# Kernel tuning notes

Measured on AMD Instinct MI355X. Metric: run time of the kernel, lower is better.

Reference implementation:

```python
import jax, jax.numpy as jnp
import numpy as np

N = 10000
E = 160000
SDIM = 256
VDIM = 128
EDIM = 32
GDIM = 32
NRBF = 20
L = 5
CUTOFF = 5.0
DIN = 2 * SDIM + NRBF + 1 + EDIM + 3 + GDIM  # 600
DOUT = SDIM + 2 * VDIM  # 512
EPS = 1e-6


def _ln(x, g, b):
    mu = jnp.mean(x, axis=-1, keepdims=True)
    var = jnp.mean((x - mu) ** 2, axis=-1, keepdims=True)
    return (x - mu) / jnp.sqrt(var + EPS) * g + b


def _vnorm(v):
    # v: [N, 3, VDIM]; divide by RMS of per-channel vector norms
    sq = jnp.sum(v * v, axis=1)  # [N, VDIM]
    f = jnp.sqrt(jnp.mean(sq, axis=-1, keepdims=True) + EPS)  # [N, 1]
    return v / f[:, :, None]


def setup_inputs() -> dict:
    key = jax.random.key(0)
    ks = jax.random.split(key, 24)
    p = jax.random.normal(ks[0], (N, 3), jnp.float32) * 2.0
    s = jax.random.normal(ks[1], (N, SDIM), jnp.float32)
    v = jnp.zeros((N, 3, VDIM), jnp.float32)
    edge_index = jax.random.randint(ks[2], (2, E), 0, N)
    src, tgt = edge_index[0], edge_index[1]
    # edge attributes exactly as in calculate_edge_attrs
    r = p[tgt] - p[src]
    edge_d = jnp.maximum(jnp.sqrt(jnp.sum(r * r, axis=-1)), 1e-6)
    pn = p / jnp.linalg.norm(p, axis=1, keepdims=True)
    edge_a = jnp.sum(pn[tgt] * pn[src], axis=-1)
    edge_rnorm = r / (1.0 + edge_d[:, None])
    edge_e = jax.random.normal(ks[3], (E, EDIM), jnp.float32) * 0.1
    edge_ohe = jax.nn.one_hot(jax.random.randint(ks[4], (E,), 0, 3), 3, dtype=jnp.float32)
    edge_global = jax.random.normal(ks[5], (E, GDIM), jnp.float32) * 0.1
    # parameters (stacked over layers)
    ln_gamma = jnp.ones((L + 1, SDIM), jnp.float32)
    ln_beta = jnp.zeros((L + 1, SDIM), jnp.float32)
    We1 = jax.random.normal(ks[6], (L, DIN, SDIM), jnp.float32) / np.sqrt(DIN)
    be1 = jnp.zeros((L, SDIM), jnp.float32)
    We2 = jax.random.normal(ks[7], (L, SDIM, DOUT), jnp.float32) / np.sqrt(SDIM)
    be2 = jnp.zeros((L, DOUT), jnp.float32)
    Wvu = jax.random.normal(ks[8], (L, VDIM, VDIM), jnp.float32) / np.sqrt(VDIM)
    Wu1 = jax.random.normal(ks[9], (L, SDIM + VDIM, SDIM), jnp.float32) / np.sqrt(SDIM + VDIM)
    bu1 = jnp.zeros((L, SDIM), jnp.float32)
    Wu2 = jax.random.normal(ks[10], (L, SDIM, SDIM + VDIM), jnp.float32) / np.sqrt(SDIM)
    bu2 = jnp.zeros((L, SDIM + VDIM), jnp.float32)
    return {"s": s, "v": v, "p": p, "edge_index": edge_index, "edge_d": edge_d,
            "edge_a": edge_a, "edge_rnorm": edge_rnorm, "edge_e": edge_e,
            "edge_ohe": edge_ohe, "edge_global": edge_global,
            "ln_gamma": ln_gamma, "ln_beta": ln_beta,
            "We1": We1, "be1": be1, "We2": We2, "be2": be2,
            "Wvu": Wvu, "Wu1": Wu1, "bu1": bu1, "Wu2": Wu2, "bu2": bu2}


def reference(s, v, p, edge_index, edge_d, edge_a, edge_rnorm, edge_e, edge_ohe,
              edge_global, ln_gamma, ln_beta, We1, be1, We2, be2, Wvu, Wu1, bu1,
              Wu2, bu2):
    src, tgt = edge_index[0], edge_index[1]
    # RBF expansion with cosine cutoff envelope
    mus = jnp.linspace(0.0, CUTOFF, NRBF).astype(s.dtype)
    coeff = -0.5 / (CUTOFF / NRBF) ** 2
    rbf = jnp.exp(coeff * (edge_d[:, None] - mus) ** 2)
    env = 0.5 * (jnp.cos(jnp.pi * edge_d / CUTOFF) + 1.0) * (edge_d < CUTOFF)
    rbf = rbf * env[:, None]  # [E, NRBF]
    cnt = jnp.maximum(jax.ops.segment_sum(jnp.ones((E,), s.dtype), tgt, num_segments=N), 1.0)[:, None]
    for i in range(L):
        s = _ln(s, ln_gamma[i], ln_beta[i])
        v = _vnorm(v)
        feat = jnp.concatenate([s[src], s[tgt], rbf, edge_a[:, None], edge_e,
                                edge_ohe, edge_global], axis=-1)  # [E, DIN]
        h = jax.nn.silu(feat @ We1[i] + be1[i])
        m = h @ We2[i] + be2[i]  # [E, DOUT]
        ms = m[:, :SDIM]
        gr = m[:, SDIM:SDIM + VDIM]
        gv = m[:, SDIM + VDIM:]
        mv = gr[:, None, :] * edge_rnorm[:, :, None] + gv[:, None, :] * v[src]  # [E,3,VDIM]
        s = s + jax.ops.segment_sum(ms, tgt, num_segments=N) / cnt
        v = v + jax.ops.segment_sum(mv, tgt, num_segments=N) / cnt[:, :, None]
        if i < L - 1:  # use_mlp_update gated-equivariant node update
            vv = jnp.einsum('ncv,vw->ncw', v, Wvu[i])
            nv = jnp.sqrt(jnp.sum(vv * vv, axis=1) + EPS)  # [N, VDIM]
            u = jax.nn.silu(jnp.concatenate([s, nv], axis=-1) @ Wu1[i] + bu1[i]) @ Wu2[i] + bu2[i]
            s = s + u[:, :SDIM]
            v = v + vv * u[:, None, SDIM:]
    s = _ln(s, ln_gamma[L], ln_beta[L])
    v = _vnorm(v)
    return (s, v, p, edge_e)
```

## Files before the change

kernel.cpp:

```cpp
#include <hip/hip_runtime.h>
#include <math.h>


constexpr int NN  = 10000;
constexpr int NE  = 160000;
constexpr int SD  = 256;
constexpr int VD  = 128;
constexpr int EFD = 88;
constexpr int DIN_ = 600;

typedef __attribute__((ext_vector_type(8))) short short8;
typedef __attribute__((ext_vector_type(4))) float f32x4;

static __device__ __forceinline__ float silu_f(float x) {
  return x / (1.0f + expf(-x));
}
static __device__ __forceinline__ ushort f2bf(float x) {
  unsigned u = __float_as_uint(x);
  unsigned r = (u + 0x7FFFu + ((u >> 16) & 1u)) >> 16;
  return (ushort)r;
}
static __device__ __forceinline__ float bf2f(ushort h) {
  return __uint_as_float(((unsigned)h) << 16);
}

__global__ __launch_bounds__(256) void k_setup(
    const float* __restrict__ edge_d, const int* __restrict__ tgt,
    float* __restrict__ rbfE, float* __restrict__ cnt)
{
  int e = blockIdx.x * 256 + threadIdx.x;
  if (e >= NE) return;
  float d = edge_d[e];
  float env = 0.0f;
  if (d < 5.0f) env = 0.5f * cosf(d * 0.628318530717958648f) + 0.5f;
  #pragma unroll
  for (int j = 0; j < 20; ++j) {
    float mu = (5.0f / 19.0f) * (float)j;
    float x = d - mu;
    rbfE[e * 20 + j] = env * expf(-8.0f * x * x);
  }
  atomicAdd(&cnt[tgt[e]], 1.0f);
}

__global__ __launch_bounds__(256) void k_invcnt(
    const float* __restrict__ cnt, float* __restrict__ icnt)
{
  int n = blockIdx.x * 256 + threadIdx.x;
  if (n < NN) icnt[n] = 1.0f / fmaxf(cnt[n], 1.0f);
}

__global__ __launch_bounds__(256) void k_scan(
    const float* __restrict__ cnt, int* __restrict__ rowstart)
{
  __shared__ float buf[256];
  __shared__ float carry_s;
  int tid = threadIdx.x;
  if (tid == 0) carry_s = 0.0f;
  __syncthreads();
  for (int base = 0; base < NN; base += 256) {
    int i = base + tid;
    float c = (i < NN) ? cnt[i] : 0.0f;
    buf[tid] = c;
    __syncthreads();
    for (int off = 1; off < 256; off <<= 1) {
      float v = (tid >= off) ? buf[tid - off] : 0.0f;
      __syncthreads();
      buf[tid] += v;
      __syncthreads();
    }
    float incl = buf[tid];
    float carry = carry_s;
    if (i < NN) rowstart[i] = (int)(carry + incl - c);
    __syncthreads();
    if (tid == 255) carry_s = carry + buf[255];
    __syncthreads();
  }
  if (tid == 0) rowstart[NN] = NE;
}

__global__ __launch_bounds__(256) void k_place(
    const int* __restrict__ src, const int* __restrict__ tgt,
    const float* __restrict__ rnorm,
    const int* __restrict__ rowstart, int* __restrict__ fill,
    int* __restrict__ eperm, int* __restrict__ src_s, int* __restrict__ tgt_s,
    float* __restrict__ rn_s)
{
  int e = blockIdx.x * 256 + threadIdx.x;
  if (e >= NE) return;
  int t = tgt[e];
  int pos = rowstart[t] + atomicAdd(&fill[t], 1);
  eperm[pos] = e;
  src_s[pos] = src[e];
  tgt_s[pos] = t;
  rn_s[pos * 4 + 0] = rnorm[(size_t)e * 3 + 0];
  rn_s[pos * 4 + 1] = rnorm[(size_t)e * 3 + 1];
  rn_s[pos * 4 + 2] = rnorm[(size_t)e * 3 + 2];
  rn_s[pos * 4 + 3] = 0.0f;
}

__global__ __launch_bounds__(256) void k_w2bf(
    const float* __restrict__ W2,
    ushort* __restrict__ wg_hi, ushort* __restrict__ wg_lo)
{
  int n = blockIdx.x, k = threadIdx.x;
  float x = W2[(size_t)k * 512 + 256 + n];
  ushort hb = f2bf(x);
  wg_hi[n * 256 + k] = hb;
  wg_lo[n * 256 + k] = f2bf(x - bf2f(hb));
}

__global__ __launch_bounds__(256) void k_wsplit(
    const float* __restrict__ W, int ldw, int K, int nbase,
    ushort* __restrict__ whi, ushort* __restrict__ wlo)
{
  int n = blockIdx.x;
  for (int k = threadIdx.x; k < K; k += 256) {
    float x = W[(size_t)k * ldw + n];
    ushort hb = f2bf(x);
    whi[(size_t)(nbase + n) * K + k] = hb;
    wlo[(size_t)(nbase + n) * K + k] = f2bf(x - bf2f(hb));
  }
}

__global__ __launch_bounds__(256) void k_ln_vnorm(
    const float* __restrict__ s, const float* __restrict__ v,
    const float* __restrict__ gamma, const float* __restrict__ beta,
    float* __restrict__ s_ln, float* __restrict__ s_copy,
    float* __restrict__ v_n, float* __restrict__ v_copy)
{
  int n = blockIdx.x, t = threadIdx.x;
  __shared__ float red[8];
  float x = s[n * SD + t];
  float ss = x, sq = x * x;
  #pragma unroll
  for (int o = 32; o > 0; o >>= 1) { ss += __shfl_down(ss, o); sq += __shfl_down(sq, o); }
  int wid = t >> 6;
  if ((t & 63) == 0) { red[wid * 2] = ss; red[wid * 2 + 1] = sq; }
  __syncthreads();
  if (t == 0) {
    float S = red[0] + red[2] + red[4] + red[6];
    float Q = red[1] + red[3] + red[5] + red[7];
    float mu = S * (1.0f / SD);
    float var = Q * (1.0f / SD) - mu * mu;
    red[0] = mu; red[1] = rsqrtf(var + 1e-6f);
  }
  __syncthreads();
  float mu = red[0], rstd = red[1];
  float y = (x - mu) * rstd * gamma[t] + beta[t];
  s_ln[n * SD + t] = y;
  if (s_copy) s_copy[n * SD + t] = y;
  __syncthreads();
  float v0 = v[n * 384 + t];
  float v1 = (t < 128) ? v[n * 384 + 256 + t] : 0.0f;
  float q = v0 * v0 + v1 * v1;
  #pragma unroll
  for (int o = 32; o > 0; o >>= 1) q += __shfl_down(q, o);
  if ((t & 63) == 0) red[wid] = q;
  __syncthreads();
  if (t == 0) red[4] = rsqrtf((red[0] + red[1] + red[2] + red[3]) * (1.0f / VD) + 1e-6f);
  __syncthreads();
  float rf = red[4];
  float w0 = v0 * rf;
  v_n[n * 384 + t] = w0;
  if (v_copy) v_copy[n * 384 + t] = w0;
  if (t < 128) {
    float w1 = v1 * rf;
    v_n[n * 384 + 256 + t] = w1;
    if (v_copy) v_copy[n * 384 + 256 + t] = w1;
  }
}

template<int DO_SILU, int SNEXT>
__global__ __launch_bounds__(256) void k_gemm_mf(
    const float* __restrict__ A, int lda,
    const ushort* __restrict__ wt_hi, const ushort* __restrict__ wt_lo,
    const float* __restrict__ bias,
    const float* __restrict__ cntf, const float* __restrict__ icnt,
    float* __restrict__ C, int ldc, int M, int K)
{
  __shared__ __align__(16) ushort Ah[64 * 40];
  __shared__ __align__(16) ushort Al[64 * 40];
  __shared__ __align__(16) ushort Bh[64 * 40];
  __shared__ __align__(16) ushort Bl[64 * 40];
  int n0 = blockIdx.x * 64;
  int m0 = blockIdx.y * 64;
  int tid = threadIdx.x;
  int srow = tid >> 2, sk8 = (tid & 3) * 8;
  int lane = tid & 63, wv = tid >> 6;
  int lg = lane >> 4, lm = lane & 15;
  f32x4 acc[4] = {};
  for (int k0 = 0; k0 < K; k0 += 32) {
    __syncthreads();
    {
      float4 a0 = make_float4(0.f, 0.f, 0.f, 0.f), a1 = a0;
      if (m0 + srow < M) {
        const float4* ap = (const float4*)&A[(size_t)(m0 + srow) * lda + k0 + sk8];
        a0 = ap[0]; a1 = ap[1];
      }
      ushort hi[8], lo[8];
      float af[8] = {a0.x, a0.y, a0.z, a0.w, a1.x, a1.y, a1.z, a1.w};
      #pragma unroll
      for (int j = 0; j < 8; ++j) {
        hi[j] = f2bf(af[j]);
        lo[j] = f2bf(af[j] - bf2f(hi[j]));
      }
      *(uint4*)&Ah[srow * 40 + sk8] = *(const uint4*)hi;
      *(uint4*)&Al[srow * 40 + sk8] = *(const uint4*)lo;
    }
    {
      *(uint4*)&Bh[srow * 40 + sk8] = *(const uint4*)&wt_hi[(size_t)(n0 + srow) * K + k0 + sk8];
      *(uint4*)&Bl[srow * 40 + sk8] = *(const uint4*)&wt_lo[(size_t)(n0 + srow) * K + k0 + sk8];
    }
    __syncthreads();
    short8 ah = *(const short8*)&Ah[(16 * wv + lm) * 40 + 8 * lg];
    short8 al = *(const short8*)&Al[(16 * wv + lm) * 40 + 8 * lg];
    #pragma unroll
    for (int cf = 0; cf < 4; ++cf) {
      short8 bh = *(const short8*)&Bh[(16 * cf + lm) * 40 + 8 * lg];
      short8 bl = *(const short8*)&Bl[(16 * cf + lm) * 40 + 8 * lg];
      acc[cf] = __builtin_amdgcn_mfma_f32_16x16x32_bf16(ah, bh, acc[cf], 0, 0, 0);
      acc[cf] = __builtin_amdgcn_mfma_f32_16x16x32_bf16(ah, bl, acc[cf], 0, 0, 0);
      acc[cf] = __builtin_amdgcn_mfma_f32_16x16x32_bf16(al, bh, acc[cf], 0, 0, 0);
    }
  }
  #pragma unroll
  for (int cf = 0; cf < 4; ++cf) {
    int col = n0 + 16 * cf + lm;
    float b = bias ? bias[col] : 0.0f;
    #pragma unroll
    for (int r = 0; r < 4; ++r) {
      int row = m0 + 16 * wv + 4 * lg + r;
      if (row >= M) continue;
      if (SNEXT) {
        C[(size_t)row * ldc + col] += (acc[cf][r] + cntf[row] * b) * icnt[row];
      } else {
        float val = acc[cf][r] + b;
        if (DO_SILU) val = silu_f(val);
        C[(size_t)row * ldc + col] = val;
      }
    }
  }
}

__global__ __launch_bounds__(256) void k_h(
    const float* __restrict__ rbfE, const float* __restrict__ edge_a,
    const float* __restrict__ edge_e, const float* __restrict__ edge_ohe,
    const float* __restrict__ edge_g,
    const int* __restrict__ eperm,
    const int* __restrict__ src_s, const int* __restrict__ tgt_s,
    const float* __restrict__ pre12,
    const float* __restrict__ W1c,
    const float* __restrict__ be1,
    int e0,
    ushort* __restrict__ h_hi, ushort* __restrict__ h_lo)
{
  __shared__ float efs[32][EFD];
  __shared__ float wc[8][SD];
  __shared__ int ep[32];
  int le0 = blockIdx.x * 32;
  int ge0 = e0 + le0;
  int tid = threadIdx.x;
  if (tid < 32) ep[tid] = eperm[ge0 + tid];
  __syncthreads();
  for (int slot = tid; slot < 32 * EFD; slot += 256) {
    int el = slot / EFD, j = slot - el * EFD;
    int e = ep[el];
    float val;
    if (j < 20)       val = rbfE[e * 20 + j];
    else if (j == 20) val = edge_a[e];
    else if (j < 53)  val = edge_e[(size_t)e * 32 + (j - 21)];
    else if (j < 56)  val = edge_ohe[(size_t)e * 3 + (j - 53)];
    else              val = edge_g[(size_t)e * 32 + (j - 56)];
    efs[el][j] = val;
  }
  int cg = tid & 15, er = tid >> 4;
  int pA = ge0 + er * 2, pB = pA + 1;
  float acc0[16] = {}, acc1[16] = {};
  for (int j0 = 0; j0 < EFD; j0 += 8) {
    __syncthreads();
    for (int sl = tid; sl < 8 * SD; sl += 256) {
      int jj = sl >> 8, c = sl & 255;
      wc[jj][c] = W1c[(j0 + jj) * SD + c];
    }
    __syncthreads();
    #pragma unroll
    for (int jj = 0; jj < 8; ++jj) {
      float a0 = efs[er * 2][j0 + jj];
      float a1 = efs[er * 2 + 1][j0 + jj];
      #pragma unroll
      for (int u = 0; u < 16; ++u) {
        float wv = wc[jj][cg + 16 * u];
        acc0[u] += a0 * wv;
        acc1[u] += a1 * wv;
      }
    }
  }
  int sA = src_s[pA], tA = tgt_s[pA], sB = src_s[pB], tB = tgt_s[pB];
  size_t hA = (size_t)(le0 + er * 2) * SD;
  #pragma unroll
  for (int u = 0; u < 16; ++u) {
    int c = cg + 16 * u;
    float b = be1[c];
    float x0 = acc0[u] + pre12[(size_t)sA * 512 + c] + pre12[(size_t)tA * 512 + 256 + c] + b;
    float x1 = acc1[u] + pre12[(size_t)sB * 512 + c] + pre12[(size_t)tB * 512 + 256 + c] + b;
    float s0 = silu_f(x0), s1 = silu_f(x1);
    ushort hb0 = f2bf(s0), hb1 = f2bf(s1);
    h_hi[hA + c]      = hb0;
    h_lo[hA + c]      = f2bf(s0 - bf2f(hb0));
    h_hi[hA + SD + c] = hb1;
    h_lo[hA + SD + c] = f2bf(s1 - bf2f(hb1));
  }
}

__global__ __launch_bounds__(256) void k_gmfma(
    const ushort* __restrict__ h_hi, const ushort* __restrict__ h_lo,
    const ushort* __restrict__ wg_hi, const ushort* __restrict__ wg_lo,
    const float* __restrict__ bias,
    float* __restrict__ g)
{
  __shared__ __align__(16) ushort Ah[64 * 40];
  __shared__ __align__(16) ushort Al[64 * 40];
  __shared__ __align__(16) ushort Bh[256 * 40];
  __shared__ __align__(16) ushort Bl[256 * 40];
  int m0 = blockIdx.x * 64;
  int tid = threadIdx.x;
  int srow = tid >> 2, sk8 = (tid & 3) * 8;
  int lane = tid & 63, wv = tid >> 6;
  int lg = lane >> 4, lm = lane & 15;
  f32x4 acc[4][4] = {};
  for (int k0 = 0; k0 < 256; k0 += 32) {
    __syncthreads();
    *(uint4*)&Ah[srow * 40 + sk8] = *(const uint4*)&h_hi[(size_t)(m0 + srow) * 256 + k0 + sk8];
    *(uint4*)&Al[srow * 40 + sk8] = *(const uint4*)&h_lo[(size_t)(m0 + srow) * 256 + k0 + sk8];
    #pragma unroll
    for (int i = 0; i < 4; ++i) {
      int task = tid + 256 * i;
      int brow = task >> 2, c8 = (task & 3) * 8;
      *(uint4*)&Bh[brow * 40 + c8] = *(const uint4*)&wg_hi[(size_t)brow * 256 + k0 + c8];
      *(uint4*)&Bl[brow * 40 + c8] = *(const uint4*)&wg_lo[(size_t)brow * 256 + k0 + c8];
    }
    __syncthreads();
    short8 ah[4], al[4];
    #pragma unroll
    for (int mf = 0; mf < 4; ++mf) {
      ah[mf] = *(const short8*)&Ah[(16 * mf + lm) * 40 + 8 * lg];
      al[mf] = *(const short8*)&Al[(16 * mf + lm) * 40 + 8 * lg];
    }
    #pragma unroll
    for (int nf = 0; nf < 4; ++nf) {
      short8 bh = *(const short8*)&Bh[(64 * wv + 16 * nf + lm) * 40 + 8 * lg];
      short8 bl = *(const short8*)&Bl[(64 * wv + 16 * nf + lm) * 40 + 8 * lg];
      #pragma unroll
      for (int mf = 0; mf < 4; ++mf) {
        acc[mf][nf] = __builtin_amdgcn_mfma_f32_16x16x32_bf16(ah[mf], bh, acc[mf][nf], 0, 0, 0);
        acc[mf][nf] = __builtin_amdgcn_mfma_f32_16x16x32_bf16(ah[mf], bl, acc[mf][nf], 0, 0, 0);
        acc[mf][nf] = __builtin_amdgcn_mfma_f32_16x16x32_bf16(al[mf], bh, acc[mf][nf], 0, 0, 0);
      }
    }
  }
  #pragma unroll
  for (int nf = 0; nf < 4; ++nf) {
    int col = 64 * wv + 16 * nf + lm;
    float b = bias[col];
    #pragma unroll
    for (int mf = 0; mf < 4; ++mf) {
      #pragma unroll
      for (int r = 0; r < 4; ++r) {
        int row = m0 + 16 * mf + 4 * lg + r;
        g[(size_t)row * 256 + col] = acc[mf][nf][r] + b;
      }
    }
  }
}

__global__ __launch_bounds__(256) void k_gather(
    const ushort* __restrict__ h_hi, const ushort* __restrict__ h_lo,
    const float* __restrict__ g,
    const int* __restrict__ rowstart,
    const int* __restrict__ src_s,
    const float* __restrict__ rn_s,
    const float* __restrict__ v_n,
    const float* __restrict__ icnt,
    int e0, int ce,
    float* __restrict__ hsum, float* __restrict__ v_next)
{
  int t = blockIdx.x;
  int lo = rowstart[t], hi = rowstart[t + 1];
  if (lo < e0) lo = e0;
  int e1 = e0 + ce;
  if (hi > e1) hi = e1;
  if (lo >= hi) return;
  int tid = threadIdx.x;
  int k = tid & 127, half = tid >> 7;
  float hacc = 0.0f, a0 = 0.0f, a1 = 0.0f, a2 = 0.0f;
  for (int p = lo; p < hi; ++p) {
    int lp = p - e0;
    hacc += bf2f(h_hi[(size_t)lp * SD + tid]) + bf2f(h_lo[(size_t)lp * SD + tid]);
    float gr = g[(size_t)lp * SD + k];
    float gv = g[(size_t)lp * SD + 128 + k];
    int sn = src_s[p];
    const float* vs = &v_n[(size_t)sn * 384];
    if (half == 0) {
      float r0 = rn_s[(size_t)p * 4 + 0];
      float r2 = rn_s[(size_t)p * 4 + 2];
      a0 += gr * r0 + gv * vs[k];
      a2 += gr * r2 + gv * vs[256 + k];
    } else {
      float r1 = rn_s[(size_t)p * 4 + 1];
      a1 += gr * r1 + gv * vs[128 + k];
    }
  }
  hsum[(size_t)t * SD + tid] += hacc;
  float ic = icnt[t];
  if (half == 0) {
    v_next[(size_t)t * 384 + k]       += ic * a0;
    v_next[(size_t)t * 384 + 256 + k] += ic * a2;
  } else {
    v_next[(size_t)t * 384 + 128 + k] += ic * a1;
  }
}

__global__ __launch_bounds__(256) void k_nv_xcat(
    const float* __restrict__ vv, const float* __restrict__ s_next,
    float* __restrict__ xcat)
{
  int n = blockIdx.x, t = threadIdx.x;
  xcat[(size_t)n * 384 + t] = s_next[(size_t)n * SD + t];
  if (t < 128) {
    float a = vv[(size_t)(n * 3 + 0) * VD + t];
    float b = vv[(size_t)(n * 3 + 1) * VD + t];
    float c = vv[(size_t)(n * 3 + 2) * VD + t];
    xcat[(size_t)n * 384 + 256 + t] = sqrtf(a * a + b * b + c * c + 1e-6f);
  }
}

__global__ __launch_bounds__(256) void k_update(
    const float* __restrict__ s_next, const float* __restrict__ v_next,
    const float* __restrict__ vv, const float* __restrict__ u,
    float* __restrict__ s_cur, float* __restrict__ v_cur)
{
  int i = blockIdx.x * 256 + threadIdx.x;
  const int NVT = NN * 384;
  if (i < NVT) {
    int n = i / 384;
    int k = (i - n * 384) & 127;
    v_cur[i] = v_next[i] + vv[i] * u[(size_t)n * 384 + 256 + k];
  } else {
    int j = i - NVT;
    if (j < NN * SD) {
      int n = j >> 8, c = j & 255;
      s_cur[j] = s_next[j] + u[(size_t)n * 384 + c];
    }
  }
}

extern "C" void kernel_launch(void* const* d_in, const int* in_sizes, int n_in,
                              void* d_out, int out_size, void* d_ws, size_t ws_size,
                              hipStream_t stream)
{
  const float* s_in   = (const float*)d_in[0];
  const float* v_in   = (const float*)d_in[1];
  const float* p_in   = (const float*)d_in[2];
  const int*   eidx   = (const int*)d_in[3];
  const float* edge_d = (const float*)d_in[4];
  const float* edge_a = (const float*)d_in[5];
  const float* rnorm  = (const float*)d_in[6];
  const float* edge_e = (const float*)d_in[7];
  const float* edge_o = (const float*)d_in[8];
  const float* edge_g = (const float*)d_in[9];
  const float* gamma  = (const float*)d_in[10];
  const float* beta   = (const float*)d_in[11];
  const float* We1    = (const float*)d_in[12];
  const float* be1    = (const float*)d_in[13];
  const float* We2    = (const float*)d_in[14];
  const float* be2    = (const float*)d_in[15];
  const float* Wvu    = (const float*)d_in[16];
  const float* Wu1    = (const float*)d_in[17];
  const float* bu1    = (const float*)d_in[18];
  const float* Wu2    = (const float*)d_in[19];
  const float* bu2    = (const float*)d_in[20];
  const int* srcA = eidx;
  const int* tgtA = eidx + NE;

  float* w = (float*)d_ws;
  float* s_cur  = w; w += NN * SD;
  float* v_cur  = w; w += NN * 384;
  float* s_ln   = w; w += NN * SD;
  float* v_nrm  = w; w += NN * 384;
  float* s_next = w; w += NN * SD;
  float* v_next = w; w += NN * 384;
  float* pre12  = w; w += NN * 512;
  float* rbfE   = w; w += (size_t)NE * 20;
  float* cnt    = w; w += NN;
  float* icnt   = w; w += NN;
  float* vv     = w; w += NN * 384;
  float* hsum   = w; w += NN * SD;
  ushort* wg_hi = (ushort*)w; w += 32768;
  ushort* wg_lo = (ushort*)w; w += 32768;
  ushort* wt_hi = (ushort*)w; w += 65536;
  ushort* wt_lo = (ushort*)w; w += 65536;
  int*   rowstart = (int*)w; w += NN + 4;
  int*   fill     = (int*)w; w += NN;
  int*   eperm    = (int*)w; w += NE;
  int*   src_s    = (int*)w; w += NE;
  int*   tgt_s    = (int*)w; w += NE;
  float* rn_s   = w; w += (size_t)NE * 4;
  float* tbuf = s_ln;
  float* ubuf = v_nrm;
  float* xcat = pre12;

  size_t fixedF = (size_t)(w - (float*)d_ws);
  size_t totalF = ws_size / sizeof(float);
  size_t availF = (totalF > fixedF) ? (totalF - fixedF) : 0;
  long long mc = (long long)(availF / 512) & ~127LL;
  if (mc > NE) mc = NE;
  if (mc < 128) mc = 128;
  const int chunkE = (int)mc;
  ushort* h_hi = (ushort*)w;
  ushort* h_lo = h_hi + (size_t)chunkE * SD;
  float*  gbuf = (float*)(h_lo + (size_t)chunkE * SD);

  hipMemsetAsync(cnt, 0, NN * sizeof(float), stream);
  hipMemsetAsync(fill, 0, NN * sizeof(int), stream);
  k_setup<<<(NE + 255) / 256, 256, 0, stream>>>(edge_d, tgtA, rbfE, cnt);
  k_scan<<<1, 256, 0, stream>>>(cnt, rowstart);
  k_invcnt<<<(NN + 255) / 256, 256, 0, stream>>>(cnt, icnt);
  k_place<<<(NE + 255) / 256, 256, 0, stream>>>(srcA, tgtA, rnorm, rowstart, fill,
                                                eperm, src_s, tgt_s, rn_s);

  const int MT = 157;
  const float* sp = s_in;
  const float* vp = v_in;
  for (int i = 0; i < 5; ++i) {
    k_ln_vnorm<<<NN, 256, 0, stream>>>(sp, vp, gamma + i * SD, beta + i * SD,
                                       s_ln, s_next, v_nrm, v_next);
    const float* W1 = We1 + (size_t)i * DIN_ * SD;
    const float* W2 = We2 + (size_t)i * SD * 512;
    k_w2bf<<<256, 256, 0, stream>>>(W2, wg_hi, wg_lo);
    k_wsplit<<<256, 256, 0, stream>>>(W1, SD, 256, 0, wt_hi, wt_lo);
    k_wsplit<<<256, 256, 0, stream>>>(W1 + 256 * SD, SD, 256, 256, wt_hi, wt_lo);
    k_gemm_mf<0, 0><<<dim3(8, MT), 256, 0, stream>>>(
        s_ln, SD, wt_hi, wt_lo, nullptr, nullptr, nullptr, pre12, 512, NN, 256);
    hipMemsetAsync(hsum, 0, (size_t)NN * SD * sizeof(float), stream);
    for (int e0 = 0; e0 < NE; e0 += chunkE) {
      int ce = NE - e0; if (ce > chunkE) ce = chunkE;
      k_h<<<ce / 32, 256, 0, stream>>>(rbfE, edge_a, edge_e, edge_o, edge_g,
                                       eperm, src_s, tgt_s, pre12, W1 + 512 * SD,
                                       be1 + i * SD, e0, h_hi, h_lo);
      k_gmfma<<<ce / 64, 256, 0, stream>>>(h_hi, h_lo, wg_hi, wg_lo,
                                           be2 + i * 512 + 256, gbuf);
      k_gather<<<NN, 256, 0, stream>>>(h_hi, h_lo, gbuf, rowstart, src_s, rn_s,
                                       v_nrm, icnt, e0, ce, hsum, v_next);
    }
    k_wsplit<<<256, 256, 0, stream>>>(W2, 512, 256, 0, wt_hi, wt_lo);
    k_gemm_mf<0, 1><<<dim3(4, MT), 256, 0, stream>>>(
        hsum, SD, wt_hi, wt_lo, be2 + i * 512, cnt, icnt, s_next, SD, NN, 256);
    if (i < 4) {
      k_wsplit<<<128, 256, 0, stream>>>(Wvu + i * VD * VD, VD, VD, 0, wt_hi, wt_lo);
      k_gemm_mf<0, 0><<<dim3(2, 469), 256, 0, stream>>>(
          v_next, VD, wt_hi, wt_lo, nullptr, nullptr, nullptr, vv, VD, 3 * NN, VD);
      k_nv_xcat<<<NN, 256, 0, stream>>>(vv, s_next, xcat);
      k_wsplit<<<256, 256, 0, stream>>>(Wu1 + (size_t)i * 384 * SD, SD, 384, 0, wt_hi, wt_lo);
      k_gemm_mf<1, 0><<<dim3(4, MT), 256, 0, stream>>>(
          xcat, 384, wt_hi, wt_lo, bu1 + i * SD, nullptr, nullptr, tbuf, SD, NN, 384);
      k_wsplit<<<384, 256, 0, stream>>>(Wu2 + (size_t)i * SD * 384, 384, 256, 0, wt_hi, wt_lo);
      k_gemm_mf<0, 0><<<dim3(6, MT), 256, 0, stream>>>(
          tbuf, SD, wt_hi, wt_lo, bu2 + i * 384, nullptr, nullptr, ubuf, 384, NN, 256);
      k_update<<<(NN * 640 + 255) / 256, 256, 0, stream>>>(s_next, v_next, vv, ubuf,
                                                           s_cur, v_cur);
      sp = s_cur; vp = v_cur;
    }
  }
  float* out = (float*)d_out;
  k_ln_vnorm<<<NN, 256, 0, stream>>>(s_next, v_next, gamma + 5 * SD, beta + 5 * SD,
                                     out, nullptr, out + NN * SD, nullptr);
  float* outp = out + (size_t)NN * SD + (size_t)NN * 384;
  hipMemcpyAsync(outp, p_in, NN * 3 * sizeof(float), hipMemcpyDeviceToDevice, stream);
  hipMemcpyAsync(outp + NN * 3, edge_e, (size_t)NE * 32 * sizeof(float),
                 hipMemcpyDeviceToDevice, stream);
}
```

Before: 3.435 ms.

## Compute edge-feature first-layer GEMM with split-bf16 MFMA on presorted edge features

Replaces the scalar FP32 edge-feature GEMM in the h kernel with a bf16 hi/lo split MFMA kernel over 64-edge tiles. Edge features (the rbf values now computed inline, plus the other edge attributes) are gathered once in sorted order and padded to 96 columns. The W1 edge slice is transposed and split per layer. This removes the per-layer irregular gathers and the FP32 FMA work. In exchange it adds a persistent bf16 edge-feature buffer and three-term bf16 precision, and it drops the rbf buffer.

```diff
diff --git a/kernel.cpp b/kernel.cpp
--- a/kernel.cpp
+++ b/kernel.cpp
@@ -6,7 +6,6 @@
 constexpr int NE  = 160000;
 constexpr int SD  = 256;
 constexpr int VD  = 128;
-constexpr int EFD = 88;
 constexpr int DIN_ = 600;
 
 typedef __attribute__((ext_vector_type(8))) short short8;
@@ -25,20 +24,10 @@
 }
 
 __global__ __launch_bounds__(256) void k_setup(
-    const float* __restrict__ edge_d, const int* __restrict__ tgt,
-    float* __restrict__ rbfE, float* __restrict__ cnt)
+    const int* __restrict__ tgt, float* __restrict__ cnt)
 {
   int e = blockIdx.x * 256 + threadIdx.x;
   if (e >= NE) return;
-  float d = edge_d[e];
-  float env = 0.0f;
-  if (d < 5.0f) env = 0.5f * cosf(d * 0.628318530717958648f) + 0.5f;
-  #pragma unroll
-  for (int j = 0; j < 20; ++j) {
-    float mu = (5.0f / 19.0f) * (float)j;
-    float x = d - mu;
-    rbfE[e * 20 + j] = env * expf(-8.0f * x * x);
-  }
   atomicAdd(&cnt[tgt[e]], 1.0f);
 }
 
@@ -96,6 +85,49 @@
   rn_s[pos * 4 + 1] = rnorm[(size_t)e * 3 + 1];
   rn_s[pos * 4 + 2] = rnorm[(size_t)e * 3 + 2];
   rn_s[pos * 4 + 3] = 0.0f;
+}
+
+__global__ __launch_bounds__(256) void k_efmat(
+    const float* __restrict__ edge_d, const float* __restrict__ edge_a,
+    const float* __restrict__ edge_e, const float* __restrict__ edge_ohe,
+    const float* __restrict__ edge_g, const int* __restrict__ eperm,
+    ushort* __restrict__ efm_hi, ushort* __restrict__ efm_lo)
+{
+  int tid = threadIdx.x;
+  int el = tid >> 3, jt = tid & 7;
+  int p = blockIdx.x * 32 + el;
+  int e = eperm[p];
+  float d = edge_d[e];
+  float env = 0.0f;
+  if (d < 5.0f) env = 0.5f * cosf(d * 0.628318530717958648f) + 0.5f;
+  #pragma unroll
+  for (int jj = 0; jj < 12; ++jj) {
+    int j = jt * 12 + jj;
+    float val;
+    if (j < 20) {
+      float x = d - (5.0f / 19.0f) * (float)j;
+      val = env * expf(-8.0f * x * x);
+    }
+    else if (j == 20) val = edge_a[e];
+    else if (j < 53)  val = edge_e[(size_t)e * 32 + (j - 21)];
+    else if (j < 56)  val = edge_ohe[(size_t)e * 3 + (j - 53)];
+    else if (j < 88)  val = edge_g[(size_t)e * 32 + (j - 56)];
+    else              val = 0.0f;
+    ushort hb = f2bf(val);
+    efm_hi[(size_t)p * 96 + j] = hb;
+    efm_lo[(size_t)p * 96 + j] = f2bf(val - bf2f(hb));
+  }
+}
+
+__global__ __launch_bounds__(96) void k_w1split(
+    const float* __restrict__ W1c,
+    ushort* __restrict__ w1t_hi, ushort* __restrict__ w1t_lo)
+{
+  int n = blockIdx.x, k = threadIdx.x;
+  float x = (k < 88) ? W1c[(size_t)k * SD + n] : 0.0f;
+  ushort hb = f2bf(x);
+  w1t_hi[n * 96 + k] = hb;
+  w1t_lo[n * 96 + k] = f2bf(x - bf2f(hb));
 }
 
 __global__ __launch_bounds__(256) void k_w2bf(
@@ -242,73 +274,97 @@
   }
 }
 
-__global__ __launch_bounds__(256) void k_h(
-    const float* __restrict__ rbfE, const float* __restrict__ edge_a,
-    const float* __restrict__ edge_e, const float* __restrict__ edge_ohe,
-    const float* __restrict__ edge_g,
-    const int* __restrict__ eperm,
+__global__ __launch_bounds__(256) void k_hmf(
+    const ushort* __restrict__ efm_hi, const ushort* __restrict__ efm_lo,
+    const ushort* __restrict__ w1t_hi, const ushort* __restrict__ w1t_lo,
+    const float* __restrict__ pre12,
     const int* __restrict__ src_s, const int* __restrict__ tgt_s,
-    const float* __restrict__ pre12,
-    const float* __restrict__ W1c,
     const float* __restrict__ be1,
     int e0,
     ushort* __restrict__ h_hi, ushort* __restrict__ h_lo)
 {
-  __shared__ float efs[32][EFD];
-  __shared__ float wc[8][SD];
-  __shared__ int ep[32];
-  int le0 = blockIdx.x * 32;
-  int ge0 = e0 + le0;
+  __shared__ __align__(16) ushort Ah[64 * 104];
+  __shared__ __align__(16) ushort Al[64 * 104];
+  __shared__ __align__(16) ushort Bh[64 * 104];
+  __shared__ __align__(16) ushort Bl[64 * 104];
+  int lb0 = blockIdx.x * 64;
+  int ge0 = e0 + lb0;
   int tid = threadIdx.x;
-  if (tid < 32) ep[tid] = eperm[ge0 + tid];
-  __syncthreads();
-  for (int slot = tid; slot < 32 * EFD; slot += 256) {
-    int el = slot / EFD, j = slot - el * EFD;
-    int e = ep[el];
-    float val;
-    if (j < 20)       val = rbfE[e * 20 + j];
-    else if (j == 20) val = edge_a[e];
-    else if (j < 53)  val = edge_e[(size_t)e * 32 + (j - 21)];
-    else if (j < 56)  val = edge_ohe[(size_t)e * 3 + (j - 53)];
-    else              val = edge_g[(size_t)e * 32 + (j - 56)];
-    efs[el][j] = val;
-  }
-  int cg = tid & 15, er = tid >> 4;
-  int pA = ge0 + er * 2, pB = pA + 1;
-  float acc0[16] = {}, acc1[16] = {};
-  for (int j0 = 0; j0 < EFD; j0 += 8) {
-    __syncthreads();
-    for (int sl = tid; sl < 8 * SD; sl += 256) {
-      int jj = sl >> 8, c = sl & 255;
-      wc[jj][c] = W1c[(j0 + jj) * SD + c];
-    }
-    __syncthreads();
-    #pragma unroll
-    for (int jj = 0; jj < 8; ++jj) {
-      float a0 = efs[er * 2][j0 + jj];
-      float a1 = efs[er * 2 + 1][j0 + jj];
+  int lane = tid & 63, wv = tid >> 6;
+  int lg = lane >> 4, lm = lane & 15;
+  #pragma unroll
+  for (int i = 0; i < 3; ++i) {
+    int task = tid + 256 * i;
+    int row = task / 12, sl = task - row * 12;
+    *(uint4*)&Ah[row * 104 + sl * 8] = *(const uint4*)&efm_hi[(size_t)(ge0 + row) * 96 + sl * 8];
+    *(uint4*)&Al[row * 104 + sl * 8] = *(const uint4*)&efm_lo[(size_t)(ge0 + row) * 96 + sl * 8];
+  }
+  int sA[4], tA[4];
+  #pragma unroll
+  for (int rr = 0; rr < 4; ++rr) {
+    int p = ge0 + 16 * wv + 4 * lg + rr;
+    sA[rr] = src_s[p];
+    tA[rr] = tgt_s[p];
+  }
+  for (int nt = 0; nt < 4; ++nt) {
+    __syncthreads();
+    #pragma unroll
+    for (int i = 0; i < 3; ++i) {
+      int task = tid + 256 * i;
+      int row = task / 12, sl = task - row * 12;
+      *(uint4*)&Bh[row * 104 + sl * 8] = *(const uint4*)&w1t_hi[(size_t)(64 * nt + row) * 96 + sl * 8];
+      *(uint4*)&Bl[row * 104 + sl * 8] = *(const uint4*)&w1t_lo[(size_t)(64 * nt + row) * 96 + sl * 8];
+    }
+    __syncthreads();
+    f32x4 acc[4] = {};
+    #pragma unroll
+    for (int ks = 0; ks < 3; ++ks) {
+      short8 ah = *(const short8*)&Ah[(16 * wv + lm) * 104 + 32 * ks + 8 * lg];
+      short8 al = *(const short8*)&Al[(16 * wv + lm) * 104 + 32 * ks + 8 * lg];
       #pragma unroll
-      for (int u = 0; u < 16; ++u) {
-        float wv = wc[jj][cg + 16 * u];
-        acc0[u] += a0 * wv;
-        acc1[u] += a1 * wv;
-      }
-    }
-  }
-  int sA = src_s[pA], tA = tgt_s[pA], sB = src_s[pB], tB = tgt_s[pB];
-  size_t hA = (size_t)(le0 + er * 2) * SD;
-  #pragma unroll
-  for (int u = 0; u < 16; ++u) {
-    int c = cg + 16 * u;
-    float b = be1[c];
-    float x0 = acc0[u] + pre12[(size_t)sA * 512 + c] + pre12[(size_t)tA * 512 + 256 + c] + b;
-    float x1 = acc1[u] + pre12[(size_t)sB * 512 + c] + pre12[(size_t)tB * 512 + 256 + c] + b;
-    float s0 = silu_f(x0), s1 = silu_f(x1);
-    ushort hb0 = f2bf(s0), hb1 = f2bf(s1);
-    h_hi[hA + c]      = hb0;
-    h_lo[hA + c]      = f2bf(s0 - bf2f(hb0));
-    h_hi[hA + SD + c] = hb1;
-    h_lo[hA + SD + c] = f2bf(s1 - bf2f(hb1));
+      for (int nf = 0; nf < 4; ++nf) {
+        short8 bh = *(const short8*)&Bh[(16 * nf + lm) * 104 + 32 * ks + 8 * lg];
+        short8 bl = *(const short8*)&Bl[(16 * nf + lm) * 104 + 32 * ks + 8 * lg];
+        acc[nf] = __builtin_amdgcn_mfma_f32_16x16x32_bf16(ah, bh, acc[nf], 0, 0, 0);
+        acc[nf] = __builtin_amdgcn_mfma_f32_16x16x32_bf16(ah, bl, acc[nf], 0, 0, 0);
+        acc[nf] = __builtin_amdgcn_mfma_f32_16x16x32_bf16(al, bh, acc[nf], 0, 0, 0);
+      }
+    }
+    ushort hh[4][4], hl[4][4];
+    #pragma unroll
+    for (int nf = 0; nf < 4; ++nf) {
+      int col = 64 * nt + 16 * nf + lm;
+      float b = be1[col];
+      #pragma unroll
+      for (int rr = 0; rr < 4; ++rr) {
+        float x = acc[nf][rr] + pre12[(size_t)sA[rr] * 512 + col]
+                + pre12[(size_t)tA[rr] * 512 + 256 + col] + b;
+        float s = silu_f(x);
+        ushort hb = f2bf(s);
+        hh[nf][rr] = hb;
+        hl[nf][rr] = f2bf(s - bf2f(hb));
+      }
+    }
+    __syncthreads();
+    #pragma unroll
+    for (int nf = 0; nf < 4; ++nf) {
+      #pragma unroll
+      for (int rr = 0; rr < 4; ++rr) {
+        int row = 16 * wv + 4 * lg + rr;
+        Bh[row * 72 + 16 * nf + lm] = hh[nf][rr];
+        Bl[row * 72 + 16 * nf + lm] = hl[nf][rr];
+      }
+    }
+    __syncthreads();
+    #pragma unroll
+    for (int i = 0; i < 2; ++i) {
+      int task = tid + 256 * i;
+      int row = task >> 3, sl = task & 7;
+      *(uint4*)&h_hi[(size_t)(lb0 + row) * 256 + 64 * nt + sl * 8] =
+          *(const uint4*)&Bh[row * 72 + sl * 8];
+      *(uint4*)&h_lo[(size_t)(lb0 + row) * 256 + 64 * nt + sl * 8] =
+          *(const uint4*)&Bl[row * 72 + sl * 8];
+    }
   }
 }
 
@@ -490,7 +546,6 @@
   float* s_next = w; w += NN * SD;
   float* v_next = w; w += NN * 384;
   float* pre12  = w; w += NN * 512;
-  float* rbfE   = w; w += (size_t)NE * 20;
   float* cnt    = w; w += NN;
   float* icnt   = w; w += NN;
   float* vv     = w; w += NN * 384;
@@ -499,6 +554,10 @@
   ushort* wg_lo = (ushort*)w; w += 32768;
   ushort* wt_hi = (ushort*)w; w += 65536;
   ushort* wt_lo = (ushort*)w; w += 65536;
+  ushort* w1t_hi = (ushort*)w; w += 12288;
+  ushort* w1t_lo = (ushort*)w; w += 12288;
+  ushort* efm_hi = (ushort*)w; w += (size_t)NE * 48;
+  ushort* efm_lo = (ushort*)w; w += (size_t)NE * 48;
   int*   rowstart = (int*)w; w += NN + 4;
   int*   fill     = (int*)w; w += NN;
   int*   eperm    = (int*)w; w += NE;
@@ -522,11 +581,13 @@
 
   hipMemsetAsync(cnt, 0, NN * sizeof(float), stream);
   hipMemsetAsync(fill, 0, NN * sizeof(int), stream);
-  k_setup<<<(NE + 255) / 256, 256, 0, stream>>>(edge_d, tgtA, rbfE, cnt);
+  k_setup<<<(NE + 255) / 256, 256, 0, stream>>>(tgtA, cnt);
   k_scan<<<1, 256, 0, stream>>>(cnt, rowstart);
   k_invcnt<<<(NN + 255) / 256, 256, 0, stream>>>(cnt, icnt);
   k_place<<<(NE + 255) / 256, 256, 0, stream>>>(srcA, tgtA, rnorm, rowstart, fill,
                                                 eperm, src_s, tgt_s, rn_s);
+  k_efmat<<<NE / 32, 256, 0, stream>>>(edge_d, edge_a, edge_e, edge_o, edge_g,
+                                       eperm, efm_hi, efm_lo);
 
   const int MT = 157;
   const float* sp = s_in;
@@ -537,6 +598,7 @@
     const float* W1 = We1 + (size_t)i * DIN_ * SD;
     const float* W2 = We2 + (size_t)i * SD * 512;
     k_w2bf<<<256, 256, 0, stream>>>(W2, wg_hi, wg_lo);
+    k_w1split<<<256, 96, 0, stream>>>(W1 + 512 * SD, w1t_hi, w1t_lo);
     k_wsplit<<<256, 256, 0, stream>>>(W1, SD, 256, 0, wt_hi, wt_lo);
     k_wsplit<<<256, 256, 0, stream>>>(W1 + 256 * SD, SD, 256, 256, wt_hi, wt_lo);
     k_gemm_mf<0, 0><<<dim3(8, MT), 256, 0, stream>>>(
@@ -544,9 +606,8 @@
     hipMemsetAsync(hsum, 0, (size_t)NN * SD * sizeof(float), stream);
     for (int e0 = 0; e0 < NE; e0 += chunkE) {
       int ce = NE - e0; if (ce > chunkE) ce = chunkE;
-      k_h<<<ce / 32, 256, 0, stream>>>(rbfE, edge_a, edge_e, edge_o, edge_g,
-                                       eperm, src_s, tgt_s, pre12, W1 + 512 * SD,
-                                       be1 + i * SD, e0, h_hi, h_lo);
+      k_hmf<<<ce / 64, 256, 0, stream>>>(efm_hi, efm_lo, w1t_hi, w1t_lo, pre12,
+                                         src_s, tgt_s, be1 + i * SD, e0, h_hi, h_lo);
       k_gmfma<<<ce / 64, 256, 0, stream>>>(h_hi, h_lo, wg_hi, wg_lo,
                                            be2 + i * 512 + 256, gbuf);
       k_gather<<<NN, 256, 0, stream>>>(h_hi, h_lo, gbuf, rowstart, src_s, rn_s,
```

Result: slower. 3.630 ms (+5.7%).
